# Kernel tuning notes

Hardware: AMD Instinct MI355X
Metric: run time of the kernel (lower is better)

## Reference

```python
import jax, jax.numpy as jnp
import numpy as np

B, S, DIM = 1, 2048, 2048
NH, NKV, HD = 32, 8, 64
NREP = NH // NKV
SCALE = 1.0 / float(np.sqrt(HD))
NEG = -1e30


def _apply_rope(q, k, rope_cache):
    # q: (B,S,NH,HD), k: (B,S,NKV,HD); rope_cache: (S, HD) = [cos | sin], each HD//2 wide
    cos = rope_cache[:, : HD // 2][None, :, None, :]  # (1,S,1,HD/2)
    sin = rope_cache[:, HD // 2 :][None, :, None, :]

    def rot(x):
        x1, x2 = x[..., : HD // 2], x[..., HD // 2 :]
        return jnp.concatenate([x1 * cos - x2 * sin, x1 * sin + x2 * cos], axis=-1)

    return rot(q), rot(k)


def setup_inputs() -> dict:
    key = jax.random.key(0)
    ks = jax.random.split(key, 12)
    std = 0.02
    x = jax.random.normal(ks[0], (B, S, DIM), jnp.float32)
    # real rotary cos/sin cache
    inv_freq = 1.0 / (10000.0 ** (np.arange(0, HD, 2, dtype=np.float64) / HD))
    freqs = np.outer(np.arange(S, dtype=np.float64), inv_freq)
    rope_cache = jnp.asarray(
        np.concatenate([np.cos(freqs), np.sin(freqs)], axis=-1), jnp.float32
    )  # (S, HD)
    return {
        "x": x,
        "rope_cache": rope_cache,
        "wq_w": jax.random.normal(ks[1], (NH * HD, DIM), jnp.float32) * std,
        "wq_b": jax.random.normal(ks[2], (NH * HD,), jnp.float32) * std,
        "wk_w": jax.random.normal(ks[3], (NKV * HD, DIM), jnp.float32) * std,
        "wk_b": jax.random.normal(ks[4], (NKV * HD,), jnp.float32) * std,
        "wv_w": jax.random.normal(ks[5], (NKV * HD, DIM), jnp.float32) * std,
        "wv_b": jax.random.normal(ks[6], (NKV * HD,), jnp.float32) * std,
        "wo_w": jax.random.normal(ks[7], (DIM, NH * HD), jnp.float32) * std,
        "wo_b": jax.random.normal(ks[8], (DIM,), jnp.float32) * std,
        "sinks": jax.random.normal(ks[9], (NH,), jnp.float32) * std,
    }


def reference(x, rope_cache, wq_w, wq_b, wk_w, wk_b, wv_w, wv_b, wo_w, wo_b, sinks):
    q = (x @ wq_w.T + wq_b).reshape(B, S, NH, HD)
    k = (x @ wk_w.T + wk_b).reshape(B, S, NKV, HD)
    v = (x @ wv_w.T + wv_b).reshape(B, S, NKV, HD)
    q, k = _apply_rope(q, k, rope_cache)
    q = q.transpose(0, 2, 1, 3)  # (B,NH,S,HD)
    k = jnp.repeat(k.transpose(0, 2, 1, 3), NREP, axis=1)  # GQA expand -> (B,NH,S,HD)
    v = jnp.repeat(v.transpose(0, 2, 1, 3), NREP, axis=1)
    scores = jnp.einsum("bhqd,bhkd->bhqk", q, k) * SCALE
    causal = jnp.tril(jnp.ones((S, S), bool))
    scores = jnp.where(causal[None, None], scores, NEG)
    lse = jax.scipy.special.logsumexp(scores, axis=-1)  # (B,NH,S)
    attn = jnp.exp(scores - lse[..., None])
    out = jnp.einsum("bhqk,bhkd->bhqd", attn, v)
    sink_scale = jax.nn.sigmoid(lse - sinks[None, :, None])  # (B,NH,S)
    out = out * sink_scale[..., None]
    out = out.transpose(0, 2, 1, 3).reshape(B, S, NH * HD)
    return out @ wo_w.T + wo_b
```

## Files before the change

kernel.cpp:

```cpp
#include <hip/hip_runtime.h>

typedef unsigned short ushort_t;
typedef short s8v __attribute__((ext_vector_type(8)));
typedef float f4v __attribute__((ext_vector_type(4)));

#define DIMK   2048
#define NHEAD  32
#define HDIM   64
#define SCALE_LOG2E 0.18033688f

__device__ __forceinline__ unsigned short f2bf(float f) {
    unsigned u = __float_as_uint(f);
    u += 0x7fffu + ((u >> 16) & 1u);
    return (unsigned short)(u >> 16);
}

__device__ __forceinline__ unsigned pack_bf2(float f0, float f1) {
    unsigned a = __float_as_uint(f0) + 0x8000u;
    unsigned b = __float_as_uint(f1) + 0x8000u;
    return __builtin_amdgcn_perm(b, a, 0x07060302u);
}

__device__ __forceinline__ float fexp2(float x) {
#if __has_builtin(__builtin_amdgcn_exp2f)
    return __builtin_amdgcn_exp2f(x);
#else
    return exp2f(x);
#endif
}

__device__ __forceinline__ void gll16(const void* g, void* l) {
    __builtin_amdgcn_global_load_lds(
        (const __attribute__((address_space(1))) void*)g,
        (__attribute__((address_space(3))) void*)l, 16, 0, 0);
}

__device__ __forceinline__ f4v mfma16(s8v a, s8v b, f4v c) {
    return __builtin_amdgcn_mfma_f32_16x16x32_bf16(a, b, c, 0, 0, 0);
}

__global__ __launch_bounds__(256) void cast_all(
    const float* __restrict__ x,  const float* __restrict__ wq,
    const float* __restrict__ wk, const float* __restrict__ wv,
    const float* __restrict__ wo,
    ushort_t* __restrict__ xb,  ushort_t* __restrict__ wqb,
    ushort_t* __restrict__ wkb, ushort_t* __restrict__ wvb,
    ushort_t* __restrict__ wob)
{
    int i = blockIdx.x * 256 + threadIdx.x;
    const float* src; ushort_t* dst;
    if      (i < 1048576) { src = x;  dst = xb; }
    else if (i < 2097152) { src = wq; dst = wqb; i -= 1048576; }
    else if (i < 2359296) { src = wk; dst = wkb; i -= 2097152; }
    else if (i < 2621440) { src = wv; dst = wvb; i -= 2359296; }
    else                  { src = wo; dst = wob; i -= 2621440; }
    float4 v = ((const float4*)src)[i];
    ushort4 o;
    o.x = f2bf(v.x); o.y = f2bf(v.y); o.z = f2bf(v.z); o.w = f2bf(v.w);
    ((ushort4*)dst)[i] = o;
}

__device__ __forceinline__ void gemm_core64(
    const ushort_t* __restrict__ A, const ushort_t* __restrict__ Bt,
    int bm, int bn64, ushort_t* As, ushort_t* Bs, f4v acc[2][4])
{
    const int tid  = threadIdx.x;
    const int wave = tid >> 6, lane = tid & 63;
    const int c = lane & 15, q4 = lane >> 4;

    const ushort_t* ag = A  + (size_t)(bm * 128 + wave * 32 + (lane >> 2)) * DIMK + (lane & 3) * 8;
    const ushort_t* bg = Bt + (size_t)(bn64 * 64 + wave * 16 + (lane >> 2)) * DIMK + (lane & 3) * 8;
    ushort_t* as0 = As + (wave * 32) * 32;
    ushort_t* as1 = As + (wave * 32 + 16) * 32;
    ushort_t* bs0 = Bs + (wave * 16) * 32;

    for (int k0 = 0; k0 < DIMK; k0 += 32) {
        gll16(ag + k0,             as0);
        gll16(ag + 16 * DIMK + k0, as1);
        gll16(bg + k0,             bs0);
        __syncthreads();
        s8v af[2], bfv[4];
#pragma unroll
        for (int mt = 0; mt < 2; ++mt)
            af[mt] = *(const s8v*)(As + (wave * 32 + mt * 16 + c) * 32 + q4 * 8);
#pragma unroll
        for (int nt = 0; nt < 4; ++nt)
            bfv[nt] = *(const s8v*)(Bs + (nt * 16 + c) * 32 + q4 * 8);
#pragma unroll
        for (int mt = 0; mt < 2; ++mt)
#pragma unroll
            for (int nt = 0; nt < 4; ++nt)
                acc[mt][nt] = mfma16(af[mt], bfv[nt], acc[mt][nt]);
        __syncthreads();
    }
}

__global__ __launch_bounds__(256) void qkv_gemm(
    const ushort_t* __restrict__ Xb,
    const ushort_t* __restrict__ Wqb, const ushort_t* __restrict__ Wkb, const ushort_t* __restrict__ Wvb,
    const float* __restrict__ biasq, const float* __restrict__ biask, const float* __restrict__ biasv,
    const float* __restrict__ rope,
    ushort_t* __restrict__ Qo, ushort_t* __restrict__ Kblk, ushort_t* __restrict__ Vblk)
{
    __shared__ ushort_t SM[8192];
    ushort_t* As = SM;
    ushort_t* Bs = SM + 4096;
    const int nb = blockIdx.x, bm = blockIdx.y;
    const ushort_t* Bt; const float* bias; int nbl, mode;
    if      (nb < 32) { Bt = Wqb; bias = biasq; nbl = nb;      mode = 0; }
    else if (nb < 40) { Bt = Wkb; bias = biask; nbl = nb - 32; mode = 1; }
    else              { Bt = Wvb; bias = biasv; nbl = nb - 40; mode = 2; }

    const f4v fz = {0.f, 0.f, 0.f, 0.f};
    f4v acc[2][4];
    for (int i = 0; i < 2; ++i) for (int j = 0; j < 4; ++j) acc[i][j] = fz;

    gemm_core64(Xb, Bt, bm, nbl, As, Bs, acc);

    const int tid = threadIdx.x, wave = tid >> 6, lane = tid & 63;
    const int c = lane & 15, q4 = lane >> 4;

    if (mode == 0) {
#pragma unroll
        for (int mt = 0; mt < 2; ++mt)
#pragma unroll
            for (int r = 0; r < 4; ++r) {
                int rowl = wave * 32 + mt * 16 + q4 * 4 + r;
                int row  = bm * 128 + rowl;
                const float* rp = rope + row * 64;
#pragma unroll
                for (int nt = 0; nt < 2; ++nt) {
                    int d   = nt * 16 + c;
                    int col = nbl * 64 + d;
                    float cs = rp[d], sn = rp[32 + d];
                    float x1 = acc[mt][nt][r]     + bias[col];
                    float x2 = acc[mt][nt + 2][r] + bias[col + 32];
                    SM[rowl * 64 + d]      = f2bf((x1 * cs - x2 * sn) * SCALE_LOG2E);
                    SM[rowl * 64 + d + 32] = f2bf((x1 * sn + x2 * cs) * SCALE_LOG2E);
                }
            }
    } else if (mode == 1) {
#pragma unroll
        for (int mt = 0; mt < 2; ++mt)
#pragma unroll
            for (int r = 0; r < 4; ++r) {
                int rowl = wave * 32 + mt * 16 + q4 * 4 + r;
                int row  = bm * 128 + rowl;
                const float* rp = rope + row * 64;
                int tl  = rowl >> 6;
                int ntk = (rowl & 63) >> 4, ck = rowl & 15;
#pragma unroll
                for (int nt = 0; nt < 2; ++nt) {
                    int d   = nt * 16 + c;
                    int col = nbl * 64 + d;
                    float cs = rp[d], sn = rp[32 + d];
                    float x1 = acc[mt][nt][r]     + bias[col];
                    float x2 = acc[mt][nt + 2][r] + bias[col + 32];
                    float o1 = x1 * cs - x2 * sn;
                    float o2 = x1 * sn + x2 * cs;
                    {   int dd = d;       int kc = dd >> 5, q4k = (dd >> 3) & 3, j = dd & 7;
                        SM[tl * 4096 + ((kc * 4 + ntk) * 64 + q4k * 16 + ck) * 8 + j] = f2bf(o1); }
                    {   int dd = d + 32;  int kc = dd >> 5, q4k = (dd >> 3) & 3, j = dd & 7;
                        SM[tl * 4096 + ((kc * 4 + ntk) * 64 + q4k * 16 + ck) * 8 + j] = f2bf(o2); }
                }
            }
    } else {
#pragma unroll
        for (int mt = 0; mt < 2; ++mt)
#pragma unroll
            for (int nt = 0; nt < 4; ++nt)
#pragma unroll
                for (int r = 0; r < 4; ++r) {
                    int rowl = wave * 32 + mt * 16 + q4 * 4 + r;
                    int col  = nbl * 64 + nt * 16 + c;
                    int tl = rowl >> 6, K64 = rowl & 63;
                    int kp = (K64 & 15) * 4 + (K64 >> 4);
                    int kc = kp >> 5, q4v = (kp >> 3) & 3, j = kp & 7;
                    SM[tl * 4096 + ((kc * 4 + nt) * 64 + q4v * 16 + c) * 8 + j]
                        = f2bf(acc[mt][nt][r] + bias[col]);
                }
    }
    __syncthreads();

    if (mode == 0) {
#pragma unroll
        for (int i = 0; i < 4; ++i) {
            int idx  = i * 256 + tid;
            int rowl = idx >> 3, c8 = (idx & 7) * 8;
            *(int4*)(Qo + (size_t)(bm * 128 + rowl) * 2048 + nbl * 64 + c8)
                = *(const int4*)(SM + idx * 8);
        }
    } else {
        ushort_t* dstb = (mode == 1 ? Kblk : Vblk) + ((size_t)nbl * 32 + bm * 2) * 4096;
#pragma unroll
        for (int i = 0; i < 4; ++i) {
            int idx = i * 256 + tid;
            *(int4*)(dstb + idx * 8) = *(const int4*)(SM + idx * 8);
        }
    }
}

__global__ __launch_bounds__(256) void proj_gemm(
    const ushort_t* __restrict__ Ob, const ushort_t* __restrict__ Wob,
    const float* __restrict__ bias, float* __restrict__ Co)
{
    __shared__ ushort_t SM[8192];
    ushort_t* As = SM;
    ushort_t* Bs = SM + 4096;
    const f4v fz = {0.f, 0.f, 0.f, 0.f};
    f4v acc[2][4];
    for (int i = 0; i < 2; ++i) for (int j = 0; j < 4; ++j) acc[i][j] = fz;

    gemm_core64(Ob, Wob, blockIdx.y, blockIdx.x, As, Bs, acc);

    const int tid = threadIdx.x, wave = tid >> 6, lane = tid & 63;
    const int c = lane & 15, q4 = lane >> 4;
#pragma unroll
    for (int mt = 0; mt < 2; ++mt)
#pragma unroll
        for (int nt = 0; nt < 4; ++nt)
#pragma unroll
            for (int r = 0; r < 4; ++r) {
                int row = blockIdx.y * 128 + wave * 32 + mt * 16 + q4 * 4 + r;
                int col = blockIdx.x * 64 + nt * 16 + c;
                Co[(size_t)row * 2048 + col] = acc[mt][nt][r] + bias[col];
            }
}

__global__ __launch_bounds__(256) void attn_kernel(
    const ushort_t* __restrict__ Qb,
    const ushort_t* __restrict__ Kblk,
    const ushort_t* __restrict__ Vblk,
    const float* __restrict__ sinks,
    ushort_t* __restrict__ Ob)
{
    __shared__ ushort_t Ps[4][32 * 72];
    const int p = blockIdx.x, h = blockIdx.y, kvh = h >> 2;
    const int tid = threadIdx.x, wave = tid >> 6, lane = tid & 63;
    const int c = lane & 15, q4 = lane >> 4;
    const int t  = (wave < 2) ? p : (31 - p);
    const int q0 = t * 64 + (wave & 1) * 32;
    ushort_t* Pw = &Ps[wave][0];

    s8v qf[2][2];
#pragma unroll
    for (int mi = 0; mi < 2; ++mi)
#pragma unroll
        for (int kc = 0; kc < 2; ++kc)
            qf[mi][kc] = *(const s8v*)(Qb + (size_t)(q0 + mi * 16 + c) * 2048 + h * 64 + kc * 32 + q4 * 8);

    const f4v fz = {0.f, 0.f, 0.f, 0.f};
    f4v Oacc[2][4];
    float Lp[2][4];
#pragma unroll
    for (int mi = 0; mi < 2; ++mi) {
#pragma unroll
        for (int dt = 0; dt < 4; ++dt) Oacc[mi][dt] = fz;
#pragma unroll
        for (int r = 0; r < 4; ++r) Lp[mi][r] = 0.f;
    }

    const ushort_t* kbase = Kblk + (size_t)kvh * 32 * 4096;
    const ushort_t* vbase = Vblk + (size_t)kvh * 32 * 4096;

    for (int kt = 0; kt <= t; ++kt) {
        const ushort_t* kp = kbase + (size_t)kt * 4096;
        const ushort_t* vp = vbase + (size_t)kt * 4096;
        s8v kf[4][2], vf[4][2];
#pragma unroll
        for (int kc = 0; kc < 2; ++kc)
#pragma unroll
            for (int nt = 0; nt < 4; ++nt) {
                kf[nt][kc] = *(const s8v*)(kp + ((kc * 4 + nt) * 64 + lane) * 8);
                vf[nt][kc] = *(const s8v*)(vp + ((kc * 4 + nt) * 64 + lane) * 8);
            }

        f4v S[2][4];
#pragma unroll
        for (int mi = 0; mi < 2; ++mi)
#pragma unroll
            for (int nt = 0; nt < 4; ++nt) S[mi][nt] = fz;
#pragma unroll
        for (int kc = 0; kc < 2; ++kc)
#pragma unroll
            for (int nt = 0; nt < 4; ++nt)
#pragma unroll
                for (int mi = 0; mi < 2; ++mi)
                    S[mi][nt] = mfma16(qf[mi][kc], kf[nt][kc], S[mi][nt]);

        if (kt == t) {
#pragma unroll
            for (int mi = 0; mi < 2; ++mi)
#pragma unroll
                for (int nt = 0; nt < 4; ++nt) {
                    int key = t * 64 + nt * 16 + c;
#pragma unroll
                    for (int r = 0; r < 4; ++r) {
                        int qrow = q0 + mi * 16 + q4 * 4 + r;
                        if (key > qrow) S[mi][nt][r] = -1.0e30f;
                    }
                }
        }

#pragma unroll
        for (int mi = 0; mi < 2; ++mi)
#pragma unroll
            for (int r = 0; r < 4; ++r) {
                float p0 = fexp2(S[mi][0][r]), p1 = fexp2(S[mi][1][r]);
                float p2 = fexp2(S[mi][2][r]), p3 = fexp2(S[mi][3][r]);
                Lp[mi][r] += (p0 + p1) + (p2 + p3);
                int2 w_; w_.x = (int)pack_bf2(p0, p1); w_.y = (int)pack_bf2(p2, p3);
                *(int2*)(Pw + (mi * 16 + q4 * 4 + r) * 72 + c * 4) = w_;
            }
        s8v pa[2][2];
#pragma unroll
        for (int mi = 0; mi < 2; ++mi)
#pragma unroll
            for (int kc = 0; kc < 2; ++kc)
                pa[mi][kc] = *(const s8v*)(Pw + (mi * 16 + c) * 72 + kc * 32 + q4 * 8);
#pragma unroll
        for (int kc = 0; kc < 2; ++kc)
#pragma unroll
            for (int dt = 0; dt < 4; ++dt)
#pragma unroll
                for (int mi = 0; mi < 2; ++mi)
                    Oacc[mi][dt] = mfma16(pa[mi][kc], vf[dt][kc], Oacc[mi][dt]);
    }

#pragma unroll
    for (int mi = 0; mi < 2; ++mi)
#pragma unroll
        for (int r = 0; r < 4; ++r)
#pragma unroll
            for (int off = 1; off < 16; off <<= 1)
                Lp[mi][r] += __shfl_xor(Lp[mi][r], off);

    const float sk = sinks[h];
#pragma unroll
    for (int mi = 0; mi < 2; ++mi)
#pragma unroll
        for (int r = 0; r < 4; ++r) {
            float L = Lp[mi][r];
            float lse = __logf(L);
            float sig = 1.f / (1.f + __expf(sk - lse));
            float sc  = sig / L;
            int row = q0 + mi * 16 + q4 * 4 + r;
#pragma unroll
            for (int dt = 0; dt < 4; ++dt)
                Ob[(size_t)row * 2048 + h * 64 + dt * 16 + c] = f2bf(Oacc[mi][dt][r] * sc);
        }
}

extern "C" void kernel_launch(void* const* d_in, const int* in_sizes, int n_in,
                              void* d_out, int out_size, void* d_ws, size_t ws_size,
                              hipStream_t stream)
{
    (void)in_sizes; (void)n_in; (void)out_size; (void)ws_size;
    const float* x     = (const float*)d_in[0];
    const float* rope  = (const float*)d_in[1];
    const float* wq    = (const float*)d_in[2];
    const float* qb    = (const float*)d_in[3];
    const float* wk    = (const float*)d_in[4];
    const float* kb    = (const float*)d_in[5];
    const float* wv    = (const float*)d_in[6];
    const float* vb    = (const float*)d_in[7];
    const float* wo    = (const float*)d_in[8];
    const float* wob_f = (const float*)d_in[9];
    const float* sinks = (const float*)d_in[10];
    float* out = (float*)d_out;

    char* ws = (char*)d_ws;
    ushort_t* xb   = (ushort_t*)(ws);
    ushort_t* wqb  = (ushort_t*)(ws + (8ull  << 20));
    ushort_t* wkb  = (ushort_t*)(ws + (16ull << 20));
    ushort_t* wvb  = (ushort_t*)(ws + (18ull << 20));
    ushort_t* wob  = (ushort_t*)(ws + (20ull << 20));
    ushort_t* qo   = (ushort_t*)(ws + (28ull << 20));
    ushort_t* kblk = (ushort_t*)(ws + (36ull << 20));
    ushort_t* vblk = (ushort_t*)(ws + (38ull << 20));
    ushort_t* ao   = (ushort_t*)(ws + (40ull << 20));

    cast_all<<<14336, 256, 0, stream>>>(x, wq, wk, wv, wo, xb, wqb, wkb, wvb, wob);
    qkv_gemm<<<dim3(48, 16), 256, 0, stream>>>(xb, wqb, wkb, wvb, qb, kb, vb, rope, qo, kblk, vblk);
    attn_kernel<<<dim3(16, 32), 256, 0, stream>>>(qo, kblk, vblk, sinks, ao);
    proj_gemm<<<dim3(32, 16), 256, 0, stream>>>(ao, wob, wob_f, out);
}
```

Measured before the change: 239.3 us.

## Double GEMM K-tile to 64 with XOR-swizzled LDS layout

The shared GEMM core now loads a 64-wide K slice per iteration instead of 32, which halves the number of barrier pairs per tile. Shared-memory rows are stored with an XOR swizzle on the 16-byte chunk index to avoid LDS bank conflicts on the MFMA fragment reads. LDS per block grows from 16KB to 24KB, which may reduce occupancy, and per-thread fragment registers double.

```diff
diff --git a/kernel.cpp b/kernel.cpp
--- a/kernel.cpp
+++ b/kernel.cpp
@@ -67,30 +67,45 @@
     const int tid  = threadIdx.x;
     const int wave = tid >> 6, lane = tid & 63;
     const int c = lane & 15, q4 = lane >> 4;
-
-    const ushort_t* ag = A  + (size_t)(bm * 128 + wave * 32 + (lane >> 2)) * DIMK + (lane & 3) * 8;
-    const ushort_t* bg = Bt + (size_t)(bn64 * 64 + wave * 16 + (lane >> 2)) * DIMK + (lane & 3) * 8;
-    ushort_t* as0 = As + (wave * 32) * 32;
-    ushort_t* as1 = As + (wave * 32 + 16) * 32;
-    ushort_t* bs0 = Bs + (wave * 16) * 32;
-
-    for (int k0 = 0; k0 < DIMK; k0 += 32) {
-        gll16(ag + k0,             as0);
-        gll16(ag + 16 * DIMK + k0, as1);
-        gll16(bg + k0,             bs0);
+    const int lrow = lane >> 3;
+    const int lchunk = (lane & 7) ^ lrow;
+
+    const ushort_t* ag = A  + (size_t)(bm * 128 + wave * 32 + lrow) * DIMK + lchunk * 8;
+    const ushort_t* bg = Bt + (size_t)(bn64 * 64 + wave * 16 + lrow) * DIMK + lchunk * 8;
+    ushort_t* asw = As + (wave * 32) * 64;
+    ushort_t* bsw = Bs + (wave * 16) * 64;
+
+    const int Ra = wave * 32 + c;
+    for (int k0 = 0; k0 < DIMK; k0 += 64) {
+        gll16(ag + k0,             asw);
+        gll16(ag +  8 * DIMK + k0, asw + 512);
+        gll16(ag + 16 * DIMK + k0, asw + 1024);
+        gll16(ag + 24 * DIMK + k0, asw + 1536);
+        gll16(bg + k0,             bsw);
+        gll16(bg +  8 * DIMK + k0, bsw + 512);
         __syncthreads();
-        s8v af[2], bfv[4];
+        s8v af[2][2], bfv[4][2];
 #pragma unroll
         for (int mt = 0; mt < 2; ++mt)
-            af[mt] = *(const s8v*)(As + (wave * 32 + mt * 16 + c) * 32 + q4 * 8);
+#pragma unroll
+            for (int kc = 0; kc < 2; ++kc) {
+                int R = Ra + mt * 16;
+                af[mt][kc] = *(const s8v*)(As + (R * 8 + ((kc * 4 + q4) ^ (R & 7))) * 8);
+            }
 #pragma unroll
         for (int nt = 0; nt < 4; ++nt)
-            bfv[nt] = *(const s8v*)(Bs + (nt * 16 + c) * 32 + q4 * 8);
-#pragma unroll
-        for (int mt = 0; mt < 2; ++mt)
-#pragma unroll
-            for (int nt = 0; nt < 4; ++nt)
-                acc[mt][nt] = mfma16(af[mt], bfv[nt], acc[mt][nt]);
+#pragma unroll
+            for (int kc = 0; kc < 2; ++kc) {
+                int R = nt * 16 + c;
+                bfv[nt][kc] = *(const s8v*)(Bs + (R * 8 + ((kc * 4 + q4) ^ (R & 7))) * 8);
+            }
+#pragma unroll
+        for (int kc = 0; kc < 2; ++kc)
+#pragma unroll
+            for (int mt = 0; mt < 2; ++mt)
+#pragma unroll
+                for (int nt = 0; nt < 4; ++nt)
+                    acc[mt][nt] = mfma16(af[mt][kc], bfv[nt][kc], acc[mt][nt]);
         __syncthreads();
     }
 }
@@ -102,9 +117,9 @@
     const float* __restrict__ rope,
     ushort_t* __restrict__ Qo, ushort_t* __restrict__ Kblk, ushort_t* __restrict__ Vblk)
 {
-    __shared__ ushort_t SM[8192];
+    __shared__ ushort_t SM[12288];
     ushort_t* As = SM;
-    ushort_t* Bs = SM + 4096;
+    ushort_t* Bs = SM + 8192;
     const int nb = blockIdx.x, bm = blockIdx.y;
     const ushort_t* Bt; const float* bias; int nbl, mode;
     if      (nb < 32) { Bt = Wqb; bias = biasq; nbl = nb;      mode = 0; }
@@ -204,9 +219,9 @@
     const ushort_t* __restrict__ Ob, const ushort_t* __restrict__ Wob,
     const float* __restrict__ bias, float* __restrict__ Co)
 {
-    __shared__ ushort_t SM[8192];
+    __shared__ ushort_t SM[12288];
     ushort_t* As = SM;
-    ushort_t* Bs = SM + 4096;
+    ushort_t* Bs = SM + 8192;
     const f4v fz = {0.f, 0.f, 0.f, 0.f};
     f4v acc[2][4];
     for (int i = 0; i < 2; ++i) for (int j = 0; j < 4; ++j) acc[i][j] = fz;
```

Measured after the change: 218.0 us. 1.1x faster.
